# Kernel optimization log

Measured on AMD Instinct MI355X. Metric: run time of the kernel, lower is better.

## Reference

```python
import jax, jax.numpy as jnp
import numpy as np
from jax import lax

BATCH, SEQ_LEN, HIDDEN, CLASSES = 512, 256, 1024, 128

def _xavier(key, shape):
    fan_out, fan_in = shape
    std = float(np.sqrt(2.0 / (fan_in + fan_out)))
    return jax.random.normal(key, shape, dtype=jnp.float32) * std

def setup_inputs() -> dict:
    key = jax.random.key(0)
    k_x, k_hx, k_hh, k_ph = jax.random.split(key, 4)
    return {
        "x": jax.random.normal(k_x, (BATCH, SEQ_LEN), dtype=jnp.float32),
        "W_hx": _xavier(k_hx, (HIDDEN, 1)),
        "W_hh": _xavier(k_hh, (HIDDEN, HIDDEN)),
        "b_h": jnp.zeros((HIDDEN,), dtype=jnp.float32),
        "W_ph": _xavier(k_ph, (CLASSES, HIDDEN)),
        "b_p": jnp.zeros((CLASSES,), dtype=jnp.float32),
    }

def reference(x, W_hx, W_hh, b_h, W_ph, b_p):
    # x: [B, T] (input_dim == 1 per timestep, as in the torch module)
    B = x.shape[0]
    H = W_hh.shape[0]
    h0 = jnp.zeros((B, H), dtype=x.dtype)

    def step(h, xt):
        # xt: [B]; xt[:, None] @ W_hx.T -> [B, H]
        h_new = jnp.tanh(xt[:, None] @ W_hx.T + h @ W_hh.T + b_h)
        return h_new, None

    h_last, _ = lax.scan(step, h0, x.T)  # scan over time: x.T is [T, B]
    # Output head applied to final hidden state (loop's last p in torch code)
    return h_last @ W_ph.T + b_p  # [B, num_classes]
```

## Files before the change

kernel.cpp:

```cpp
#include <hip/hip_runtime.h>
#include <stdint.h>


#define BATCH 512
#define SEQ   256
#define HID   1024
#define CLS   128

#define GB 32
#define GJ 8
#define BT 16
#define JT 128
#define HSTR 132
#define HS_OFF 16384
#define SMEM_BYTES (32768 + BT * HSTR * 2)
#define HBUF_HALVES (BATCH * HID)

typedef __attribute__((ext_vector_type(8))) short  bf16x8;
typedef __attribute__((ext_vector_type(4))) short  s16x4;
typedef __attribute__((ext_vector_type(4))) float  f32x4;
typedef __attribute__((ext_vector_type(4))) int    i32x4;
typedef __attribute__((ext_vector_type(2))) unsigned int u32x2;

__device__ __forceinline__ unsigned short f2bf(float f) {
  unsigned int u = __float_as_uint(f);
  u = (u + 0x7FFFu + ((u >> 16) & 1u)) >> 16;
  return (unsigned short)u;
}
__device__ __forceinline__ float b2f(short h) {
  return __uint_as_float(((unsigned int)(unsigned short)h) << 16);
}

__device__ __forceinline__ void store_flag(int* p, int v) {
  asm volatile("global_store_dword %0, %1, off sc0 sc1" :: "v"(p), "v"(v) : "memory");
}
__device__ __forceinline__ int load_flag(const int* p) {
  int v;
  asm volatile("global_load_dword %0, %1, off sc0 sc1\n\t"
               "s_waitcnt vmcnt(0)" : "=v"(v) : "v"(p) : "memory");
  return v;
}
__device__ __forceinline__ void store16(void* p, i32x4 v) {
  asm volatile("global_store_dwordx4 %0, %1, off sc0 sc1" :: "v"(p), "v"(v) : "memory");
}
__device__ __forceinline__ void waitcnt0() {
  asm volatile("s_waitcnt vmcnt(0)" ::: "memory");
}
__device__ __forceinline__ void barrier_lgkm() {
  asm volatile("s_waitcnt lgkmcnt(0)\n\ts_barrier" ::: "memory");
}
__device__ __forceinline__ void issue4_64(const void* p, i32x4& a, i32x4& b, i32x4& c, i32x4& d) {
  asm volatile(
    "global_load_dwordx4 %0, %4, off sc0 sc1\n\t"
    "global_load_dwordx4 %1, %4, off offset:64 sc0 sc1\n\t"
    "global_load_dwordx4 %2, %4, off offset:128 sc0 sc1\n\t"
    "global_load_dwordx4 %3, %4, off offset:192 sc0 sc1"
    : "=&v"(a), "=&v"(b), "=&v"(c), "=&v"(d)
    : "v"(p) : "memory");
}
__device__ __forceinline__ void issue4_16(const void* p, i32x4& a, i32x4& b, i32x4& c, i32x4& d) {
  asm volatile(
    "global_load_dwordx4 %0, %4, off sc0 sc1\n\t"
    "global_load_dwordx4 %1, %4, off offset:16 sc0 sc1\n\t"
    "global_load_dwordx4 %2, %4, off offset:32 sc0 sc1\n\t"
    "global_load_dwordx4 %3, %4, off offset:48 sc0 sc1"
    : "=&v"(a), "=&v"(b), "=&v"(c), "=&v"(d)
    : "v"(p) : "memory");
}

__device__ __forceinline__ void wr16(short* p, i32x4 v) {
  u32x2 lo, hi;
  lo.x = (unsigned)v.x; lo.y = (unsigned)v.y;
  hi.x = (unsigned)v.z; hi.y = (unsigned)v.w;
  *(u32x2*)p = lo;
  *(u32x2*)(p + 4) = hi;
}
__device__ __forceinline__ float tanh_fast(float z) {
  float e = __expf(2.f * z);
  return 1.f - 2.f / (e + 1.f);
}

#define MFMA(a, b, c) __builtin_amdgcn_mfma_f32_16x16x32_bf16((a), (b), (c), 0, 0, 0)

__global__ void __launch_bounds__(256, 1)
rnn_persistent(const float* __restrict__ x, const float* __restrict__ Whx,
               const float* __restrict__ Whh, const float* __restrict__ bh,
               const float* __restrict__ Wph, const float* __restrict__ bp,
               float* __restrict__ out, unsigned short* hbuf, int* flags)
{
  extern __shared__ short smem[];
  float* scr = (float*)smem;
  short* hS  = smem + HS_OFF;

  const int tid  = threadIdx.x;
  const int bg   = blockIdx.x & 31;
  const int jg   = blockIdx.x >> 5;
  const int lane = tid & 63;
  const int wv   = tid >> 6;
  const int l15  = lane & 15;
  const int quad = lane >> 4;

  bf16x8 barr[8][8];
#pragma unroll
  for (int ct = 0; ct < 8; ++ct) {
#pragma unroll
    for (int ks = 0; ks < 8; ++ks) {
      const float* wp = Whh + (jg * JT + ct * 16 + l15) * HID
                            + wv * 256 + ks * 32 + quad * 8;
      float4 fA = *(const float4*)(wp);
      float4 fB = *(const float4*)(wp + 4);
      union { bf16x8 v8; s16x4 h[2]; } u;
      u.h[0].x = (short)f2bf(fA.x); u.h[0].y = (short)f2bf(fA.y);
      u.h[0].z = (short)f2bf(fA.z); u.h[0].w = (short)f2bf(fA.w);
      u.h[1].x = (short)f2bf(fB.x); u.h[1].y = (short)f2bf(fB.y);
      u.h[1].z = (short)f2bf(fB.z); u.h[1].w = (short)f2bf(fB.w);
      barr[ct][ks] = u.v8;
    }
  }

  const int j0 = jg * JT + wv * 32 + l15;
  const int j1 = j0 + 16;
  const float whx0 = Whx[j0], whx1 = Whx[j1];
  const float bhv0 = bh[j0],  bhv1 = bh[j1];

  const int sr  = tid >> 4;
  const int seg = tid & 15;

  int* myflags = flags + bg * 64;

  for (int t = 0; t < SEQ; ++t) {
    const unsigned short* hin = hbuf + ((t + 1) & 1) * HBUF_HALVES;
    unsigned short*      hout = hbuf + (t & 1) * HBUF_HALVES;

    f32x4 acc0 = {0,0,0,0}, acc1 = {0,0,0,0}, acc2 = {0,0,0,0}, acc3 = {0,0,0,0};
    f32x4 acc4 = {0,0,0,0}, acc5 = {0,0,0,0}, acc6 = {0,0,0,0}, acc7 = {0,0,0,0};

    float xv[4];
    {
      const float* xp = x + (bg * BT + quad * 4) * SEQ + t;
#pragma unroll
      for (int rg = 0; rg < 4; ++rg) xv[rg] = xp[rg * SEQ];
    }

    if (t > 0) {
      if (tid < GJ) {
        while (load_flag(myflags + tid) < t) {
          asm volatile("s_sleep 1" ::: "memory");
        }
      }
      __syncthreads();

      const short* pA = (const short*)hin + (bg * BT + l15) * HID
                        + wv * 256 + quad * 8;
      i32x4 A0, A1, A2, A3, A4, A5, A6, A7;
      issue4_64(pA,       A0, A1, A2, A3);
      issue4_64(pA + 128, A4, A5, A6, A7);

      asm volatile("s_waitcnt vmcnt(0)"
                   : "+v"(A0), "+v"(A1), "+v"(A2), "+v"(A3),
                     "+v"(A4), "+v"(A5), "+v"(A6), "+v"(A7)
                   :: "memory");
      __builtin_amdgcn_sched_barrier(0);

#define KSTEP(Ar, KS) { \
      bf16x8 _a = *(const bf16x8*)&(Ar); \
      acc0 = MFMA(_a, barr[0][KS], acc0); acc1 = MFMA(_a, barr[1][KS], acc1); \
      acc2 = MFMA(_a, barr[2][KS], acc2); acc3 = MFMA(_a, barr[3][KS], acc3); \
      acc4 = MFMA(_a, barr[4][KS], acc4); acc5 = MFMA(_a, barr[5][KS], acc5); \
      acc6 = MFMA(_a, barr[6][KS], acc6); acc7 = MFMA(_a, barr[7][KS], acc7); }
      KSTEP(A0, 0) KSTEP(A1, 1) KSTEP(A2, 2) KSTEP(A3, 3)
      KSTEP(A4, 4) KSTEP(A5, 5) KSTEP(A6, 6) KSTEP(A7, 7)
#undef KSTEP
    }

    barrier_lgkm();
#pragma unroll
    for (int ct = 0; ct < 8; ++ct) {
      f32x4 w = (ct == 0) ? acc0 : (ct == 1) ? acc1 : (ct == 2) ? acc2 :
                (ct == 3) ? acc3 : (ct == 4) ? acc4 : (ct == 5) ? acc5 :
                (ct == 6) ? acc6 : acc7;
      *(f32x4*)(scr + ((ct * 4 + wv) * 64 + lane) * 4) = w;
    }
    barrier_lgkm();
    {
      f32x4 f0 = {0,0,0,0}, f1 = {0,0,0,0};
#pragma unroll
      for (int w = 0; w < 4; ++w) {
        f0 += *(const f32x4*)(scr + (((2 * wv)     * 4 + w) * 64 + lane) * 4);
        f1 += *(const f32x4*)(scr + (((2 * wv + 1) * 4 + w) * 64 + lane) * 4);
      }
#pragma unroll
      for (int rg = 0; rg < 4; ++rg) {
        float z0 = f0[rg] + xv[rg] * whx0 + bhv0;
        hS[(quad * 4 + rg) * HSTR + wv * 32 + l15] = (short)f2bf(tanh_fast(z0));
        float z1 = f1[rg] + xv[rg] * whx1 + bhv1;
        hS[(quad * 4 + rg) * HSTR + wv * 32 + 16 + l15] = (short)f2bf(tanh_fast(z1));
      }
    }
    barrier_lgkm();
    {
      const short* hsrc = hS + sr * HSTR + seg * 8;
      u32x2 lo = *(const u32x2*)(hsrc);
      u32x2 hi = *(const u32x2*)(hsrc + 4);
      i32x4 sv; sv.x = (int)lo.x; sv.y = (int)lo.y; sv.z = (int)hi.x; sv.w = (int)hi.y;
      unsigned short* dst = hout + (bg * BT + sr) * HID + jg * JT + seg * 8;
      store16(dst, sv);
    }
    waitcnt0();
    barrier_lgkm();
    if (tid == 0) store_flag(myflags + jg, t + 1);
  }

  if (tid < GJ) {
    while (load_flag(myflags + tid) < SEQ) {
      asm volatile("s_sleep 1" ::: "memory");
    }
  }
  __syncthreads();

  const unsigned short* hlast = hbuf + ((SEQ - 1) & 1) * HBUF_HALVES;
  {
    const char* lbase = (const char*)(hlast + (bg * BT + sr) * HID) + seg * 128;
    i32x4 p0, p1, p2, p3, p4, p5, p6, p7;
    issue4_16(lbase,      p0, p1, p2, p3);
    issue4_16(lbase + 64, p4, p5, p6, p7);
    waitcnt0();
    short* sdst = smem + sr * 1028 + seg * 64;
    wr16(sdst,      p0); wr16(sdst + 8,  p1); wr16(sdst + 16, p2); wr16(sdst + 24, p3);
    wr16(sdst + 32, p4); wr16(sdst + 40, p5); wr16(sdst + 48, p6); wr16(sdst + 56, p7);
  }
  __syncthreads();
  {
    const int hr = tid >> 4;
    const int cc = tid & 15;
    const int cg = jg * 16 + cc;
    const float* wp = Wph + cg * HID;
    const short* hs = smem + hr * 1028;
    float acc = 0.f;
#pragma unroll 8
    for (int k4 = 0; k4 < 256; ++k4) {
      float4 w  = *(const float4*)(wp + k4 * 4);
      s16x4 hv  = *(const s16x4*)(hs + k4 * 4);
      acc += b2f(hv.x) * w.x + b2f(hv.y) * w.y + b2f(hv.z) * w.z + b2f(hv.w) * w.w;
    }
    out[(bg * BT + hr) * CLS + cg] = acc + bp[cg];
  }
}

extern "C" void kernel_launch(void* const* d_in, const int* in_sizes, int n_in,
                              void* d_out, int out_size, void* d_ws, size_t ws_size,
                              hipStream_t stream) {
  const float* x   = (const float*)d_in[0];
  const float* Whx = (const float*)d_in[1];
  const float* Whh = (const float*)d_in[2];
  const float* bh  = (const float*)d_in[3];
  const float* Wph = (const float*)d_in[4];
  const float* bp  = (const float*)d_in[5];
  float* out = (float*)d_out;

  unsigned short* hbuf = (unsigned short*)d_ws;
  int* flags = (int*)((char*)d_ws + (size_t)2 * HBUF_HALVES * 2);

  hipMemsetAsync(flags, 0, GB * 64 * sizeof(int), stream);

  hipFuncSetAttribute(reinterpret_cast<const void*>(rnn_persistent),
                      hipFuncAttributeMaxDynamicSharedMemorySize, SMEM_BYTES);

  rnn_persistent<<<dim3(GB * GJ), dim3(256), SMEM_BYTES, stream>>>(
      x, Whx, Whh, bh, Wph, bp, out, hbuf, flags);
}
```

Baseline: 966.0 us.

## Replace per-step flag synchronization with parity tags embedded in hidden-state data

Removes the global flag array and the per-step store-wait-barrier-flag handshake. The LSB of every eighth bf16 hidden value now carries a parity tag for the timestep, and readers spin-reload their operand loads until all tags match. This takes a full round-trip flag poll and two block barriers off the critical path of each recurrent step. In exchange it perturbs the low mantissa bit of some hidden values, and it relies on 16-byte stores becoming visible atomically and on the 0xFF memset of the whole buffer before launch.

```diff
diff --git a/kernel.cpp b/kernel.cpp
--- a/kernel.cpp
+++ b/kernel.cpp
@@ -31,15 +31,6 @@
   return __uint_as_float(((unsigned int)(unsigned short)h) << 16);
 }
 
-__device__ __forceinline__ void store_flag(int* p, int v) {
-  asm volatile("global_store_dword %0, %1, off sc0 sc1" :: "v"(p), "v"(v) : "memory");
-}
-__device__ __forceinline__ int load_flag(const int* p) {
-  int v;
-  asm volatile("global_load_dword %0, %1, off sc0 sc1\n\t"
-               "s_waitcnt vmcnt(0)" : "=v"(v) : "v"(p) : "memory");
-  return v;
-}
 __device__ __forceinline__ void store16(void* p, i32x4 v) {
   asm volatile("global_store_dwordx4 %0, %1, off sc0 sc1" :: "v"(p), "v"(v) : "memory");
 }
@@ -67,6 +58,10 @@
     : "=&v"(a), "=&v"(b), "=&v"(c), "=&v"(d)
     : "v"(p) : "memory");
 }
+#define TIED_WAIT8(A0,A1,A2,A3,A4,A5,A6,A7) \
+  asm volatile("s_waitcnt vmcnt(0)" \
+               : "+v"(A0), "+v"(A1), "+v"(A2), "+v"(A3), \
+                 "+v"(A4), "+v"(A5), "+v"(A6), "+v"(A7) :: "memory")
 
 __device__ __forceinline__ void wr16(short* p, i32x4 v) {
   u32x2 lo, hi;
@@ -79,6 +74,13 @@
   float e = __expf(2.f * z);
   return 1.f - 2.f / (e + 1.f);
 }
+__device__ __forceinline__ bool stale8(const i32x4& a, const i32x4& b,
+                                       const i32x4& c, const i32x4& d,
+                                       const i32x4& e, const i32x4& f,
+                                       const i32x4& g, const i32x4& h, int tg) {
+  return ((((a.x ^ tg) | (b.x ^ tg) | (c.x ^ tg) | (d.x ^ tg) |
+            (e.x ^ tg) | (f.x ^ tg) | (g.x ^ tg) | (h.x ^ tg)) & 1)) != 0;
+}
 
 #define MFMA(a, b, c) __builtin_amdgcn_mfma_f32_16x16x32_bf16((a), (b), (c), 0, 0, 0)
 
@@ -86,7 +88,7 @@
 rnn_persistent(const float* __restrict__ x, const float* __restrict__ Whx,
                const float* __restrict__ Whh, const float* __restrict__ bh,
                const float* __restrict__ Wph, const float* __restrict__ bp,
-               float* __restrict__ out, unsigned short* hbuf, int* flags)
+               float* __restrict__ out, unsigned short* hbuf)
 {
   extern __shared__ short smem[];
   float* scr = (float*)smem;
@@ -122,15 +124,16 @@
   const int j1 = j0 + 16;
   const float whx0 = Whx[j0], whx1 = Whx[j1];
   const float bhv0 = bh[j0],  bhv1 = bh[j1];
+  const int tagger = (l15 & 7) == 0;
 
   const int sr  = tid >> 4;
   const int seg = tid & 15;
-
-  int* myflags = flags + bg * 64;
 
   for (int t = 0; t < SEQ; ++t) {
     const unsigned short* hin = hbuf + ((t + 1) & 1) * HBUF_HALVES;
     unsigned short*      hout = hbuf + (t & 1) * HBUF_HALVES;
+    const int tg_w = (t >> 1) & 1;
+    const int tg_r = ((t - 1) >> 1) & 1;
 
     f32x4 acc0 = {0,0,0,0}, acc1 = {0,0,0,0}, acc2 = {0,0,0,0}, acc3 = {0,0,0,0};
     f32x4 acc4 = {0,0,0,0}, acc5 = {0,0,0,0}, acc6 = {0,0,0,0}, acc7 = {0,0,0,0};
@@ -143,23 +146,20 @@
     }
 
     if (t > 0) {
-      if (tid < GJ) {
-        while (load_flag(myflags + tid) < t) {
-          asm volatile("s_sleep 1" ::: "memory");
-        }
-      }
-      __syncthreads();
-
       const short* pA = (const short*)hin + (bg * BT + l15) * HID
                         + wv * 256 + quad * 8;
       i32x4 A0, A1, A2, A3, A4, A5, A6, A7;
       issue4_64(pA,       A0, A1, A2, A3);
       issue4_64(pA + 128, A4, A5, A6, A7);
-
-      asm volatile("s_waitcnt vmcnt(0)"
-                   : "+v"(A0), "+v"(A1), "+v"(A2), "+v"(A3),
-                     "+v"(A4), "+v"(A5), "+v"(A6), "+v"(A7)
-                   :: "memory");
+      TIED_WAIT8(A0, A1, A2, A3, A4, A5, A6, A7);
+      if (__builtin_expect(stale8(A0, A1, A2, A3, A4, A5, A6, A7, tg_r), 0)) {
+        do {
+          asm volatile("s_sleep 32" ::: "memory");
+          issue4_64(pA,       A0, A1, A2, A3);
+          issue4_64(pA + 128, A4, A5, A6, A7);
+          TIED_WAIT8(A0, A1, A2, A3, A4, A5, A6, A7);
+        } while (stale8(A0, A1, A2, A3, A4, A5, A6, A7, tg_r));
+      }
       __builtin_amdgcn_sched_barrier(0);
 
 #define KSTEP(Ar, KS) { \
@@ -191,10 +191,14 @@
       }
 #pragma unroll
       for (int rg = 0; rg < 4; ++rg) {
-        float z0 = f0[rg] + xv[rg] * whx0 + bhv0;
-        hS[(quad * 4 + rg) * HSTR + wv * 32 + l15] = (short)f2bf(tanh_fast(z0));
-        float z1 = f1[rg] + xv[rg] * whx1 + bhv1;
-        hS[(quad * 4 + rg) * HSTR + wv * 32 + 16 + l15] = (short)f2bf(tanh_fast(z1));
+        unsigned short v0 = f2bf(tanh_fast(f0[rg] + xv[rg] * whx0 + bhv0));
+        unsigned short v1 = f2bf(tanh_fast(f1[rg] + xv[rg] * whx1 + bhv1));
+        if (tagger) {
+          v0 = (unsigned short)((v0 & 0xFFFEu) | (unsigned)tg_w);
+          v1 = (unsigned short)((v1 & 0xFFFEu) | (unsigned)tg_w);
+        }
+        hS[(quad * 4 + rg) * HSTR + wv * 32 + l15]      = (short)v0;
+        hS[(quad * 4 + rg) * HSTR + wv * 32 + 16 + l15] = (short)v1;
       }
     }
     barrier_lgkm();
@@ -206,25 +210,26 @@
       unsigned short* dst = hout + (bg * BT + sr) * HID + jg * JT + seg * 8;
       store16(dst, sv);
     }
-    waitcnt0();
-    barrier_lgkm();
-    if (tid == 0) store_flag(myflags + jg, t + 1);
-  }
-
-  if (tid < GJ) {
-    while (load_flag(myflags + tid) < SEQ) {
-      asm volatile("s_sleep 1" ::: "memory");
-    }
-  }
-  __syncthreads();
+  }
+
+  barrier_lgkm();
 
   const unsigned short* hlast = hbuf + ((SEQ - 1) & 1) * HBUF_HALVES;
+  const int tg_l = ((SEQ - 1) >> 1) & 1;
   {
     const char* lbase = (const char*)(hlast + (bg * BT + sr) * HID) + seg * 128;
     i32x4 p0, p1, p2, p3, p4, p5, p6, p7;
     issue4_16(lbase,      p0, p1, p2, p3);
     issue4_16(lbase + 64, p4, p5, p6, p7);
-    waitcnt0();
+    TIED_WAIT8(p0, p1, p2, p3, p4, p5, p6, p7);
+    if (stale8(p0, p1, p2, p3, p4, p5, p6, p7, tg_l)) {
+      do {
+        asm volatile("s_sleep 32" ::: "memory");
+        issue4_16(lbase,      p0, p1, p2, p3);
+        issue4_16(lbase + 64, p4, p5, p6, p7);
+        TIED_WAIT8(p0, p1, p2, p3, p4, p5, p6, p7);
+      } while (stale8(p0, p1, p2, p3, p4, p5, p6, p7, tg_l));
+    }
     short* sdst = smem + sr * 1028 + seg * 64;
     wr16(sdst,      p0); wr16(sdst + 8,  p1); wr16(sdst + 16, p2); wr16(sdst + 24, p3);
     wr16(sdst + 32, p4); wr16(sdst + 40, p5); wr16(sdst + 48, p6); wr16(sdst + 56, p7);
@@ -259,13 +264,12 @@
   float* out = (float*)d_out;
 
   unsigned short* hbuf = (unsigned short*)d_ws;
-  int* flags = (int*)((char*)d_ws + (size_t)2 * HBUF_HALVES * 2);
-
-  hipMemsetAsync(flags, 0, GB * 64 * sizeof(int), stream);
+
+  hipMemsetAsync(d_ws, 0xFF, (size_t)2 * HBUF_HALVES * 2, stream);
 
   hipFuncSetAttribute(reinterpret_cast<const void*>(rnn_persistent),
                       hipFuncAttributeMaxDynamicSharedMemorySize, SMEM_BYTES);
 
   rnn_persistent<<<dim3(GB * GJ), dim3(256), SMEM_BYTES, stream>>>(
-      x, Whx, Whh, bh, Wph, bp, out, hbuf, flags);
-}
+      x, Whx, Whh, bh, Wph, bp, out, hbuf);
+}
```

After: 1.026 ms. 1.06x slower.
